# Optimization experiments

Measured on AMD Instinct MI355X. Metric: run time of the kernel, lower is better.

The kernel has to match this reference:

```python
import jax, jax.numpy as jnp
import numpy as np

WIDTH = 384
STEP_SIZE = 0.1  # hard-coded in EnergyBlock.__init__
EPS = 1e-5


def conv1d(x, w):
    # x: [B, Cin, L], w: [Cout, Cin, K], stride 1, SAME padding (padding=1 for k=3)
    return jax.lax.conv_general_dilated(
        x, w, window_strides=(1,), padding='SAME',
        dimension_numbers=('NCH', 'OIH', 'NCH'))


def layer_norm_cl(x):
    # torch layer_norm over shape[1:] == normalize jointly over (C, L) per batch elem,
    # no affine params, biased variance.
    mu = jnp.mean(x, axis=(1, 2), keepdims=True)
    var = jnp.mean(jnp.square(x - mu), axis=(1, 2), keepdims=True)
    return (x - mu) * jax.lax.rsqrt(var + EPS)


def energy_block(cat, op_w):
    # cat: [B, width+1, L] = concat(interim_thought, x)
    xl = layer_norm_cl(cat[:, :WIDTH])          # post-LN x (the grad variable)
    c = conv1d(cat, op_w)                        # operator(inputs): no path through xl
    # Ex = sum(c * xl) + sum(where(xl>=0, xl^2, 0))
    # dEx/dxl = c + 2*relu(xl)  (analytic; matches torch.autograd.grad)
    grads = c + 2.0 * jnp.maximum(xl, 0.0)
    return xl - STEP_SIZE * grads


def _init_conv(key, cout, cin, k=3):
    scale = (1.0 / (cin * k)) ** 0.5
    return jax.random.uniform(key, (cout, cin, k), jnp.float32, -scale, scale)


def setup_inputs() -> dict:
    key = jax.random.key(0)
    ks = jax.random.split(key, 6)
    B, L = 32, 512
    return {
        'x': jax.random.normal(ks[0], (B, 1, L), jnp.float32),
        'iters_to_do': 16,
        'proj_w': _init_conv(ks[1], WIDTH, 1),
        'op_w': _init_conv(ks[2], WIDTH, WIDTH + 1),
        'h1_w': _init_conv(ks[3], WIDTH, WIDTH),
        'h2_w': _init_conv(ks[4], WIDTH // 2, WIDTH),
        'h3_w': _init_conv(ks[5], 2, WIDTH // 2),
    }


def reference(x, iters_to_do, proj_w, op_w, h1_w, h2_w, h3_w):
    relu = jax.nn.relu
    interim = relu(conv1d(x, proj_w))  # initial_thought [B, width, L]

    def step(it, _):
        cat = jnp.concatenate([it, x], axis=1)       # recall=True
        new_it = energy_block(cat, op_w)
        out = conv1d(relu(conv1d(relu(conv1d(new_it, h1_w)), h2_w)), h3_w)  # [B,2,L]
        return new_it, out

    _, outs = jax.lax.scan(step, interim, None, length=iters_to_do)
    # eval mode: return all_outputs [B, iters, 2, L]
    return jnp.transpose(outs, (1, 0, 2, 3))
```

## Files before the change

### kernel.cpp

```cpp
#include <hip/hip_runtime.h>
#include <hip/hip_bf16.h>

#define BB 32
#define WW 384
#define LL 512
#define ITERS 16
#define NPB (WW * LL)
#define LROWS 514
#define RP (LROWS * 8)

typedef __attribute__((ext_vector_type(8))) short bf16x8;
typedef __attribute__((ext_vector_type(4))) float f32x4;

__device__ __forceinline__ float b2f(short s) {
    unsigned u = ((unsigned)(unsigned short)s) << 16;
    float f;
    __builtin_memcpy(&f, &u, 4);
    return f;
}
__device__ __forceinline__ short f2b(float v) {
    __hip_bfloat16 h = __float2bfloat16(v);
    return *(short*)&h;
}

__device__ __forceinline__ void gld16(const short* g, short* l) {
    __builtin_amdgcn_global_load_lds(
        (const __attribute__((address_space(1))) unsigned int*)g,
        (__attribute__((address_space(3))) unsigned int*)l, 16, 0, 0);
}

__global__ __launch_bounds__(256) void prep(
    const float* __restrict__ op_w, const float* __restrict__ h1_w,
    const float* __restrict__ h2_w, short* __restrict__ wOph,
    short* __restrict__ wH1, short* __restrict__ wH2, float* __restrict__ wx,
    short* itAh, short* itAl, short* itBh, short* itBl,
    short* a1A, short* a1B, short* a2A, short* a2B, float* part) {
    int bid = blockIdx.x, tid = threadIdx.x;
    if (bid < 1728) {
        int i = bid * 256 + tid;
        int e = i & 7, co = (i >> 3) % 384, oct = (i >> 3) / 384 % 48,
            tap = i / (8 * 384 * 48);
        wOph[i] = f2b(op_w[(co * 385 + oct * 8 + e) * 3 + tap]);
    } else if (bid < 3456) {
        int i = (bid - 1728) * 256 + tid;
        int e = i & 7, co = (i >> 3) % 384, oct = (i >> 3) / 384 % 48,
            tap = i / (8 * 384 * 48);
        wH1[i] = f2b(h1_w[(co * 384 + oct * 8 + e) * 3 + tap]);
    } else if (bid < 4320) {
        int i = (bid - 3456) * 256 + tid;
        int e = i & 7, co = (i >> 3) % 192, oct = (i >> 3) / 192 % 48,
            tap = i / (8 * 192 * 48);
        wH2[i] = f2b(h2_w[(co * 384 + oct * 8 + e) * 3 + tap]);
    } else if (bid < 4325) {
        int i = (bid - 4320) * 256 + tid;
        if (i < 3 * 384) {
            int co = i % 384, tap = i / 384;
            wx[tap * 384 + co] = op_w[(co * 385 + 384) * 3 + tap];
        }
    } else if (bid < 4330) {
        int i = (bid - 4325) * 256 + tid;
        if (i < (ITERS + 1) * 64) part[i] = 0.f;
    } else {
        int rb = bid - 4330;
        int row = (rb & 1) ? (LROWS - 1) : 0;
        int b = rb >> 1;
        for (int i = tid; i < 48 * 8; i += 256) {
            size_t o = (size_t)b * 48 * RP + (size_t)(i >> 3) * RP +
                       row * 8 + (i & 7);
            itAh[o] = 0; itAl[o] = 0; itBh[o] = 0; itBl[o] = 0;
            a1A[o] = 0; a1B[o] = 0;
        }
        for (int i = tid; i < 24 * 8; i += 256) {
            size_t o = (size_t)b * 24 * RP + (size_t)(i >> 3) * RP +
                       row * 8 + (i & 7);
            a2A[o] = 0; a2B[o] = 0;
        }
    }
}

__global__ __launch_bounds__(256) void proj_relu(const float* __restrict__ x,
                                                 const float* __restrict__ wp,
                                                 short* __restrict__ oh,
                                                 short* __restrict__ ol,
                                                 float* __restrict__ part) {
    int low3 = blockIdx.x & 7, r0 = blockIdx.x >> 3;
    int sl_lo = r0 & 3, chi = r0 >> 2;
    int c3 = chi * 8 + low3;
    int b = c3 >> 1, sl = ((c3 & 1) << 2) | sl_lo;
    int tid = threadIdx.x;
    __shared__ float ws[WW * 3];
    __shared__ float xs[66];
    for (int i = tid; i < WW * 3; i += 256) ws[i] = wp[i];
    int l0 = sl * 64;
    for (int i = tid; i < 66; i += 256) {
        int l = l0 + i - 1;
        xs[i] = (l >= 0 && l < LL) ? x[b * LL + l] : 0.f;
    }
    __syncthreads();
    size_t sb = (size_t)b * 48 * RP;
    float s = 0.f, sq = 0.f;
    for (int idx = tid; idx < 64 * WW; idx += 256) {
        int lo = idx / WW, co = idx % WW;
        float v = fmaxf(ws[co * 3] * xs[lo] + ws[co * 3 + 1] * xs[lo + 1] +
                            ws[co * 3 + 2] * xs[lo + 2], 0.f);
        size_t o = sb + (size_t)(co >> 3) * RP + (l0 + lo + 1) * 8 + (co & 7);
        __hip_bfloat16 h = __float2bfloat16(v);
        oh[o] = *(short*)&h;
        ol[o] = f2b(v - __bfloat162float(h));
        s += v; sq += v * v;
    }
    #pragma unroll
    for (int off = 32; off > 0; off >>= 1) {
        s += __shfl_down(s, off);
        sq += __shfl_down(sq, off);
    }
    __shared__ float sr[8];
    int w = tid >> 6;
    if ((tid & 63) == 0) { sr[w] = s; sr[4 + w] = sq; }
    __syncthreads();
    if (tid == 0) {
        atomicAdd(&part[b * 2], sr[0] + sr[1] + sr[2] + sr[3]);
        atomicAdd(&part[b * 2 + 1], sr[4] + sr[5] + sr[6] + sr[7]);
    }
}


#define PIPE_BARRIER()                                                     \
    do {                                                                   \
        asm volatile("s_waitcnt vmcnt(8)" ::: "memory");                   \
        __builtin_amdgcn_sched_barrier(0);                                 \
        __builtin_amdgcn_s_barrier();                                      \
        __builtin_amdgcn_sched_barrier(0);                                 \
    } while (0)

#define MMAC(A, B, MT, NT)                                                 \
    acc[MT][NT] = __builtin_amdgcn_mfma_f32_16x16x32_bf16(A, B,            \
                                                          acc[MT][NT], 0, 0, 0);

#define STAGE_R(KG, TB, S0, S1)                                            \
    do {                                                                   \
        short* sb_ = smem + (TB) * ASZ;                                    \
        _Pragma("unroll")                                                  \
        for (int r_ = 0; r_ < ((S1) - (S0) + 3) / 4; r_++) {               \
            int s_ = (S0) + r_ * 4 + wn;                                   \
            if (s_ < (S1)) {                                               \
                int u0_ = s_ * 64;                                         \
                if (u0_ > AU - 64) u0_ = AU - 64;                          \
                int u_ = u0_ + lane;                                       \
                int oc_ = u_ / TLROWS;                                     \
                int rw_ = u_ - oc_ * TLROWS;                               \
                gld16(inh + ibase + (size_t)((KG) * GOCT + oc_) * RP +     \
                          (size_t)(l0 + rw_) * 8,                          \
                      sb_ + u0_ * 8);                                      \
            }                                                              \
        }                                                                  \
    } while (0)

#define DECL_B(S) bf16x8 fb0##S, fb1##S, fb2##S, fb3##S;

#define LOADB(S, T, KC)                                                    \
    do {                                                                   \
        const short* bp_ = wh + ((((size_t)(T) * CHUNKS + (KC)) * 4 + q) * \
                                     COD + co0w + lane15) * 8;             \
        fb0##S = *(const bf16x8*)(bp_);                                    \
        fb1##S = *(const bf16x8*)(bp_ + 16 * 8);                           \
        fb2##S = *(const bf16x8*)(bp_ + 32 * 8);                           \
        fb3##S = *(const bf16x8*)(bp_ + 48 * 8);                           \
    } while (0)

#define COMP_TAP(SB, OG, T, S)                                             \
    do {                                                                   \
        const short* As_ = (SB);                                           \
        int ar_ = ((OG) * 4 + q) * TLROWS + wl + lane15 + (T);             \
        bf16x8 fa0 = *(const bf16x8*)(As_ + ar_ * 8);                      \
        bf16x8 fa1 = *(const bf16x8*)(As_ + (ar_ + 16) * 8);               \
        bf16x8 fa2 = *(const bf16x8*)(As_ + (ar_ + 32) * 8);               \
        bf16x8 fa3 = *(const bf16x8*)(As_ + (ar_ + 48) * 8);               \
        MMAC(fa0, fb0##S, 0, 0) MMAC(fa0, fb1##S, 0, 1)                    \
        MMAC(fa0, fb2##S, 0, 2) MMAC(fa0, fb3##S, 0, 3)                    \
        MMAC(fa1, fb0##S, 1, 0) MMAC(fa1, fb1##S, 1, 1)                    \
        MMAC(fa1, fb2##S, 1, 2) MMAC(fa1, fb3##S, 1, 3)                    \
        MMAC(fa2, fb0##S, 2, 0) MMAC(fa2, fb1##S, 2, 1)                    \
        MMAC(fa2, fb2##S, 2, 2) MMAC(fa2, fb3##S, 2, 3)                    \
        MMAC(fa3, fb0##S, 3, 0) MMAC(fa3, fb1##S, 3, 1)                    \
        MMAC(fa3, fb2##S, 3, 2) MMAC(fa3, fb3##S, 3, 3)                    \
    } while (0)

template <int CHUNKS, int IOCT, int OOCT, int COD, int MODE, int LSPLIT,
          int GOCT>
__device__ __forceinline__ void conv_body(
    int bid, short* smem,
    const short* __restrict__ inh, const short* __restrict__ inl,
    const short* __restrict__ wh, const float* __restrict__ xf,
    const float* __restrict__ wx, const float* __restrict__ part_in,
    float* __restrict__ part_out, short* __restrict__ outh,
    short* __restrict__ outl) {
    constexpr int TLROWS = LSPLIT ? 258 : 130;
    constexpr int SUBS = GOCT / 4;
    constexpr int NG = CHUNKS / SUBS;
    constexpr int ASZ = GOCT * TLROWS * 8;
    constexpr int AU = GOCT * TLROWS;
    constexpr int ANS = (AU + 63) / 64;
    constexpr int SPS = (ANS + SUBS - 1) / SUBS;

    int tid = threadIdx.x;
    int lane = tid & 63;
    int wn = __builtin_amdgcn_readfirstlane(tid >> 6);
    int lane15 = lane & 15, q = lane >> 4;
    int b, l0, co0, wl, wco;
    if (LSPLIT) {
        int low3 = bid & 7, r0 = bid >> 3;
        int ct = r0 % 3, chi = r0 / 3;
        int c2 = chi * 8 + low3;
        b = c2 >> 1; l0 = (c2 & 1) * 256; co0 = ct * 64;
        wl = wn * 64; wco = 0;
    } else {
        int low3 = bid & 7, r0 = bid >> 3;
        int ct = r0 % 3, s2 = r0 / 3;
        int ltlo = s2 & 1, chi = s2 >> 1;
        int c = chi * 8 + low3;
        b = c >> 1;
        int lt = ((c & 1) << 1) | ltlo;
        l0 = lt * 128; co0 = ct * 128;
        wl = (wn >> 1) * 64; wco = (wn & 1) * 64;
    }
    const int co0w = co0 + wco;
    const size_t ibase = (size_t)b * IOCT * RP;

    f32x4 acc[4][4];
    #pragma unroll
    for (int i = 0; i < 4; i++)
        #pragma unroll
        for (int j = 0; j < 4; j++) acc[i][j] = (f32x4){0.f, 0.f, 0.f, 0.f};

    DECL_B(X)
    DECL_B(Y)
    DECL_B(Z)
    STAGE_R(0, 0, 0, ANS);
    LOADB(X, 0, 0);
    LOADB(Y, 1, 0);
    PIPE_BARRIER();
    #pragma unroll 2
    for (int g = 0; g < NG; g++) {
        int cur = g & 1;
        short* sb = smem + cur * ASZ;
        #pragma unroll
        for (int s = 0; s < SUBS; s++) {
            int kc = g * SUBS + s;
            LOADB(Z, 2, kc);
            if (g + 1 < NG) {
                int s0 = s * SPS;
                int s1 = (s0 + SPS > ANS) ? ANS : s0 + SPS;
                STAGE_R(g + 1, cur ^ 1, s0, s1);
            }
            COMP_TAP(sb, s, 0, X);
            if (kc + 1 < CHUNKS) LOADB(X, 0, kc + 1);
            COMP_TAP(sb, s, 1, Y);
            if (kc + 1 < CHUNKS) LOADB(Y, 1, kc + 1);
            COMP_TAP(sb, s, 2, Z);
        }
        PIPE_BARRIER();
    }

    int l0w = l0 + wl;
    const size_t obase = (size_t)b * OOCT * RP;
    if constexpr (MODE == 1) {
        float s_in = part_in[b * 2], sq_in = part_in[b * 2 + 1];
        float mu = s_in / (float)NPB;
        float var = sq_in / (float)NPB - mu * mu;
        float rs = rsqrtf(var + 1e-5f);
        const float* xb = xf + b * LL;
        float s = 0.f, sq = 0.f;
        #pragma unroll
        for (int nt = 0; nt < 4; nt++) {
            int n = co0w + nt * 16 + lane15;
            float w0 = wx[n], w1 = wx[384 + n], w2 = wx[768 + n];
            #pragma unroll
            for (int mt = 0; mt < 4; mt++)
                #pragma unroll
                for (int r = 0; r < 4; r++) {
                    int m = mt * 16 + q * 4 + r;
                    int l = l0w + m;
                    size_t idx = ibase + (size_t)(n >> 3) * RP +
                                 (l + 1) * 8 + (n & 7);
                    float xm1 = (l > 0) ? xb[l - 1] : 0.f;
                    float xp1 = (l < LL - 1) ? xb[l + 1] : 0.f;
                    float c = acc[mt][nt][r] + w0 * xm1 + w1 * xb[l] + w2 * xp1;
                    float itv = b2f(inh[idx]) + b2f(inl[idx]);
                    float xl = (itv - mu) * rs;
                    float nv = xl - 0.1f * c - 0.2f * fmaxf(xl, 0.f);
                    s += nv;
                    sq += nv * nv;
                    __hip_bfloat16 h = __float2bfloat16(nv);
                    outh[idx] = *(short*)&h;
                    outl[idx] = f2b(nv - __bfloat162float(h));
                }
        }
        #pragma unroll
        for (int off = 32; off > 0; off >>= 1) {
            s += __shfl_down(s, off);
            sq += __shfl_down(sq, off);
        }
        __shared__ float sr[8];
        if (lane == 0) { sr[wn] = s; sr[4 + wn] = sq; }
        __syncthreads();
        if (tid == 0) {
            atomicAdd(&part_out[b * 2], sr[0] + sr[1] + sr[2] + sr[3]);
            atomicAdd(&part_out[b * 2 + 1], sr[4] + sr[5] + sr[6] + sr[7]);
        }
    } else {
        #pragma unroll
        for (int mt = 0; mt < 4; mt++)
            #pragma unroll
            for (int nt = 0; nt < 4; nt++)
                #pragma unroll
                for (int r = 0; r < 4; r++) {
                    int m = mt * 16 + q * 4 + r;
                    int n = co0w + nt * 16 + lane15;
                    size_t idx = obase + (size_t)(n >> 3) * RP +
                                 (l0w + m + 1) * 8 + (n & 7);
                    outh[idx] = f2b(fmaxf(acc[mt][nt][r], 0.f));
                }
    }
}

__device__ __forceinline__ void h3_body(int bid, short* smem,
                                        const short* __restrict__ a2,
                                        const float* __restrict__ w3,
                                        float* __restrict__ out, int t) {
    float* ws3 = (float*)smem;
    int tid = threadIdx.x;
    for (int i = tid; i < 2 * 192 * 3; i += 256) ws3[i] = w3[i];
    __syncthreads();
    int low3 = bid & 7, r0 = bid >> 3;
    int qlo = r0 & 1, chi = r0 >> 1;
    int c = chi * 8 + low3;
    int b = c >> 1;
    int qq = ((c & 1) << 1) | qlo;
    int l = qq * 128 + (tid >> 1);
    int ch = tid & 1;
    const short* ab = a2 + (size_t)b * 24 * RP;
    const float* wc = ws3 + ch * 576;
    float a = 0.f;
    #pragma unroll 4
    for (int oct = 0; oct < 24; oct++) {
        const short* p = ab + (size_t)oct * RP + l * 8;
        bf16x8 v0 = *(const bf16x8*)p;
        bf16x8 v1 = *(const bf16x8*)(p + 8);
        bf16x8 v2 = *(const bf16x8*)(p + 16);
        #pragma unroll
        for (int j = 0; j < 8; j++) {
            const float* wp = wc + (oct * 8 + j) * 3;
            a += wp[0] * b2f(v0[j]) + wp[1] * b2f(v1[j]) + wp[2] * b2f(v2[j]);
        }
    }
    out[(((size_t)b * ITERS + t) * 2 + ch) * LL + l] = a;
}

__global__ __launch_bounds__(256, 3) void fusedF(
    const short* __restrict__ ch, const short* __restrict__ cl,
    short* __restrict__ nh, short* __restrict__ nl,
    const short* __restrict__ wOph, const short* __restrict__ wH1,
    const short* __restrict__ wH2, const float* __restrict__ xf,
    const float* __restrict__ wx, const float* __restrict__ part_in,
    float* __restrict__ part_out, short* __restrict__ a1w,
    const short* __restrict__ a1r, short* __restrict__ a2w,
    const short* __restrict__ a2r, const float* __restrict__ w3,
    float* __restrict__ out, int th3, int opB, int h1B, int h2B) {
    __shared__ __align__(16) short smem[2 * 8 * 130 * 8];
    int bid = blockIdx.x;
    if (bid < opB) {
        conv_body<12, 48, 48, 384, 1, 0, 8>(bid, smem, ch, cl, wOph, xf, wx,
                                            part_in, part_out, nh, nl);
    } else if (bid < opB + h1B) {
        conv_body<12, 48, 48, 384, 0, 0, 8>(bid - opB, smem, ch, nullptr,
                                            wH1, nullptr, nullptr, nullptr,
                                            nullptr, a1w, nullptr);
    } else if (bid < opB + h1B + h2B) {
        conv_body<12, 48, 24, 192, 0, 1, 4>(bid - opB - h1B, smem, a1r,
                                            nullptr, wH2, nullptr, nullptr,
                                            nullptr, nullptr, a2w, nullptr);
    } else {
        h3_body(bid - opB - h1B - h2B, smem, a2r, w3, out, th3);
    }
}

extern "C" void kernel_launch(void* const* d_in, const int* in_sizes, int n_in,
                              void* d_out, int out_size, void* d_ws, size_t ws_size,
                              hipStream_t stream) {
    const float* x = (const float*)d_in[0];
    const float* proj_w = (const float*)d_in[2];
    const float* op_w = (const float*)d_in[3];
    const float* h1_w = (const float*)d_in[4];
    const float* h2_w = (const float*)d_in[5];
    const float* h3_w = (const float*)d_in[6];
    float* out = (float*)d_out;

    char* base = (char*)d_ws;
    size_t off = 0;
    auto alloc = [&](size_t bytes) {
        char* p = base + off;
        off += (bytes + 255) & ~(size_t)255;
        return p;
    };
    const size_t ITB = (size_t)BB * 48 * RP * 2;
    short* itAh = (short*)alloc(ITB);
    short* itAl = (short*)alloc(ITB);
    short* itBh = (short*)alloc(ITB);
    short* itBl = (short*)alloc(ITB);
    short* a1A = (short*)alloc((size_t)BB * 48 * RP * 2);
    short* a1B = (short*)alloc((size_t)BB * 48 * RP * 2);
    short* a2A = (short*)alloc((size_t)BB * 24 * RP * 2);
    short* a2B = (short*)alloc((size_t)BB * 24 * RP * 2);
    short* wOph = (short*)alloc((size_t)3 * 48 * 384 * 8 * 2);
    short* wH1 = (short*)alloc((size_t)3 * 48 * 384 * 8 * 2);
    short* wH2 = (short*)alloc((size_t)3 * 48 * 192 * 8 * 2);
    float* wx = (float*)alloc((size_t)3 * 384 * 4);
    float* part = (float*)alloc((size_t)(ITERS + 1) * 64 * 4);
    if (off > ws_size) return;

    prep<<<4394, 256, 0, stream>>>(op_w, h1_w, h2_w, wOph, wH1, wH2, wx,
                                   itAh, itAl, itBh, itBl, a1A, a1B, a2A,
                                   a2B, part);
    proj_relu<<<BB * 8, 256, 0, stream>>>(x, proj_w, itAh, itAl, part);

    short* a1buf[2] = {a1A, a1B};
    short* a2buf[2] = {a2A, a2B};
    short *ch = itAh, *cl = itAl, *nh = itBh, *nl = itBl;
    for (int t = 0; t < ITERS + 3; t++) {
        int opB = (t < ITERS) ? 384 : 0;
        int h1B = (t >= 1 && t <= ITERS) ? 384 : 0;
        int h2B = (t >= 2 && t <= ITERS + 1) ? 192 : 0;
        int h3B = (t >= 3 && t <= ITERS + 2) ? 128 : 0;
        int tp = (t < ITERS) ? t : 0;
        fusedF<<<opB + h1B + h2B + h3B, 256, 0, stream>>>(
            ch, cl, nh, nl, wOph, wH1, wH2, x, wx, part + tp * 64,
            part + (tp + 1) * 64, a1buf[(t - 1) & 1], a1buf[(t - 2) & 1],
            a2buf[(t - 2) & 1], a2buf[(t + 1) & 1], h3_w, out, t - 3,
            opB, h1B, h2B);
        if (t < ITERS) {
            short* th = ch; ch = nh; nh = th;
            short* tl = cl; cl = nl; nl = tl;
        }
    }
}
```

Baseline: 940.4 us.

## Shrink LDS staging to 4-octet chunks and unify h2 tiling with op/h1

```diff
diff --git a/kernel.cpp b/kernel.cpp
--- a/kernel.cpp
+++ b/kernel.cpp
@@ -137,19 +137,19 @@
     acc[MT][NT] = __builtin_amdgcn_mfma_f32_16x16x32_bf16(A, B,            \
                                                           acc[MT][NT], 0, 0, 0);
 
-#define STAGE_R(KG, TB, S0, S1)                                            \
+#define STAGE(KC, TB)                                                      \
     do {                                                                   \
         short* sb_ = smem + (TB) * ASZ;                                    \
         _Pragma("unroll")                                                  \
-        for (int r_ = 0; r_ < ((S1) - (S0) + 3) / 4; r_++) {               \
-            int s_ = (S0) + r_ * 4 + wn;                                   \
-            if (s_ < (S1)) {                                               \
+        for (int r_ = 0; r_ < 3; r_++) {                                   \
+            int s_ = r_ * 4 + wn;                                          \
+            if (s_ < 9) {                                                  \
                 int u0_ = s_ * 64;                                         \
                 if (u0_ > AU - 64) u0_ = AU - 64;                          \
                 int u_ = u0_ + lane;                                       \
                 int oc_ = u_ / TLROWS;                                     \
                 int rw_ = u_ - oc_ * TLROWS;                               \
-                gld16(inh + ibase + (size_t)((KG) * GOCT + oc_) * RP +     \
+                gld16(inh + ibase + (size_t)((KC) * 4 + oc_) * RP +        \
                           (size_t)(l0 + rw_) * 8,                          \
                       sb_ + u0_ * 8);                                      \
             }                                                              \
@@ -168,10 +168,10 @@
         fb3##S = *(const bf16x8*)(bp_ + 48 * 8);                           \
     } while (0)
 
-#define COMP_TAP(SB, OG, T, S)                                             \
+#define COMP_TAP(SB, T, S)                                                 \
     do {                                                                   \
         const short* As_ = (SB);                                           \
-        int ar_ = ((OG) * 4 + q) * TLROWS + wl + lane15 + (T);             \
+        int ar_ = q * TLROWS + wl + lane15 + (T);                          \
         bf16x8 fa0 = *(const bf16x8*)(As_ + ar_ * 8);                      \
         bf16x8 fa1 = *(const bf16x8*)(As_ + (ar_ + 16) * 8);               \
         bf16x8 fa2 = *(const bf16x8*)(As_ + (ar_ + 32) * 8);               \
@@ -186,8 +186,8 @@
         MMAC(fa3, fb2##S, 3, 2) MMAC(fa3, fb3##S, 3, 3)                    \
     } while (0)
 
-template <int CHUNKS, int IOCT, int OOCT, int COD, int MODE, int LSPLIT,
-          int GOCT>
+template <int CHUNKS, int IOCT, int OOCT, int COD, int MODE, int NCT,
+          int CSTR>
 __device__ __forceinline__ void conv_body(
     int bid, short* smem,
     const short* __restrict__ inh, const short* __restrict__ inl,
@@ -195,35 +195,22 @@
     const float* __restrict__ wx, const float* __restrict__ part_in,
     float* __restrict__ part_out, short* __restrict__ outh,
     short* __restrict__ outl) {
-    constexpr int TLROWS = LSPLIT ? 258 : 130;
-    constexpr int SUBS = GOCT / 4;
-    constexpr int NG = CHUNKS / SUBS;
-    constexpr int ASZ = GOCT * TLROWS * 8;
-    constexpr int AU = GOCT * TLROWS;
-    constexpr int ANS = (AU + 63) / 64;
-    constexpr int SPS = (ANS + SUBS - 1) / SUBS;
+    constexpr int TLROWS = 130;
+    constexpr int ASZ = 4 * TLROWS * 8;
+    constexpr int AU = 4 * TLROWS;
 
     int tid = threadIdx.x;
     int lane = tid & 63;
     int wn = __builtin_amdgcn_readfirstlane(tid >> 6);
     int lane15 = lane & 15, q = lane >> 4;
-    int b, l0, co0, wl, wco;
-    if (LSPLIT) {
-        int low3 = bid & 7, r0 = bid >> 3;
-        int ct = r0 % 3, chi = r0 / 3;
-        int c2 = chi * 8 + low3;
-        b = c2 >> 1; l0 = (c2 & 1) * 256; co0 = ct * 64;
-        wl = wn * 64; wco = 0;
-    } else {
-        int low3 = bid & 7, r0 = bid >> 3;
-        int ct = r0 % 3, s2 = r0 / 3;
-        int ltlo = s2 & 1, chi = s2 >> 1;
-        int c = chi * 8 + low3;
-        b = c >> 1;
-        int lt = ((c & 1) << 1) | ltlo;
-        l0 = lt * 128; co0 = ct * 128;
-        wl = (wn >> 1) * 64; wco = (wn & 1) * 64;
-    }
+    int low3 = bid & 7, r0 = bid >> 3;
+    int ct = r0 % NCT, s2 = r0 / NCT;
+    int ltlo = s2 & 1, chi = s2 >> 1;
+    int c = chi * 8 + low3;
+    int b = c >> 1;
+    int lt = ((c & 1) << 1) | ltlo;
+    int l0 = lt * 128, co0 = ct * CSTR;
+    int wl = (wn >> 1) * 64, wco = (wn & 1) * 64;
     const int co0w = co0 + wco;
     const size_t ibase = (size_t)b * IOCT * RP;
 
@@ -236,29 +223,21 @@
     DECL_B(X)
     DECL_B(Y)
     DECL_B(Z)
-    STAGE_R(0, 0, 0, ANS);
+    STAGE(0, 0);
     LOADB(X, 0, 0);
     LOADB(Y, 1, 0);
     PIPE_BARRIER();
     #pragma unroll 2
-    for (int g = 0; g < NG; g++) {
-        int cur = g & 1;
+    for (int kc = 0; kc < CHUNKS; kc++) {
+        int cur = kc & 1;
+        LOADB(Z, 2, kc);
+        if (kc + 1 < CHUNKS) STAGE(kc + 1, cur ^ 1);
         short* sb = smem + cur * ASZ;
-        #pragma unroll
-        for (int s = 0; s < SUBS; s++) {
-            int kc = g * SUBS + s;
-            LOADB(Z, 2, kc);
-            if (g + 1 < NG) {
-                int s0 = s * SPS;
-                int s1 = (s0 + SPS > ANS) ? ANS : s0 + SPS;
-                STAGE_R(g + 1, cur ^ 1, s0, s1);
-            }
-            COMP_TAP(sb, s, 0, X);
-            if (kc + 1 < CHUNKS) LOADB(X, 0, kc + 1);
-            COMP_TAP(sb, s, 1, Y);
-            if (kc + 1 < CHUNKS) LOADB(Y, 1, kc + 1);
-            COMP_TAP(sb, s, 2, Z);
-        }
+        COMP_TAP(sb, 0, X);
+        if (kc + 1 < CHUNKS) LOADB(X, 0, kc + 1);
+        COMP_TAP(sb, 1, Y);
+        if (kc + 1 < CHUNKS) LOADB(Y, 1, kc + 1);
+        COMP_TAP(sb, 2, Z);
         PIPE_BARRIER();
     }
 
@@ -285,10 +264,11 @@
                                  (l + 1) * 8 + (n & 7);
                     float xm1 = (l > 0) ? xb[l - 1] : 0.f;
                     float xp1 = (l < LL - 1) ? xb[l + 1] : 0.f;
-                    float c = acc[mt][nt][r] + w0 * xm1 + w1 * xb[l] + w2 * xp1;
+                    float c2 = acc[mt][nt][r] + w0 * xm1 + w1 * xb[l] +
+                               w2 * xp1;
                     float itv = b2f(inh[idx]) + b2f(inl[idx]);
                     float xl = (itv - mu) * rs;
-                    float nv = xl - 0.1f * c - 0.2f * fmaxf(xl, 0.f);
+                    float nv = xl - 0.1f * c2 - 0.2f * fmaxf(xl, 0.f);
                     s += nv;
                     sq += nv * nv;
                     __hip_bfloat16 h = __float2bfloat16(nv);
@@ -357,7 +337,7 @@
     out[(((size_t)b * ITERS + t) * 2 + ch) * LL + l] = a;
 }
 
-__global__ __launch_bounds__(256, 3) void fusedF(
+__global__ __launch_bounds__(256, 4) void fusedF(
     const short* __restrict__ ch, const short* __restrict__ cl,
     short* __restrict__ nh, short* __restrict__ nl,
     const short* __restrict__ wOph, const short* __restrict__ wH1,
@@ -367,19 +347,19 @@
     const short* __restrict__ a1r, short* __restrict__ a2w,
     const short* __restrict__ a2r, const float* __restrict__ w3,
     float* __restrict__ out, int th3, int opB, int h1B, int h2B) {
-    __shared__ __align__(16) short smem[2 * 8 * 130 * 8];
+    __shared__ __align__(16) short smem[2 * 4 * 130 * 8];
     int bid = blockIdx.x;
     if (bid < opB) {
-        conv_body<12, 48, 48, 384, 1, 0, 8>(bid, smem, ch, cl, wOph, xf, wx,
-                                            part_in, part_out, nh, nl);
+        conv_body<12, 48, 48, 384, 1, 3, 128>(bid, smem, ch, cl, wOph, xf,
+                                              wx, part_in, part_out, nh, nl);
     } else if (bid < opB + h1B) {
-        conv_body<12, 48, 48, 384, 0, 0, 8>(bid - opB, smem, ch, nullptr,
-                                            wH1, nullptr, nullptr, nullptr,
-                                            nullptr, a1w, nullptr);
+        conv_body<12, 48, 48, 384, 0, 3, 128>(bid - opB, smem, ch, nullptr,
+                                              wH1, nullptr, nullptr, nullptr,
+                                              nullptr, a1w, nullptr);
     } else if (bid < opB + h1B + h2B) {
-        conv_body<12, 48, 24, 192, 0, 1, 4>(bid - opB - h1B, smem, a1r,
-                                            nullptr, wH2, nullptr, nullptr,
-                                            nullptr, nullptr, a2w, nullptr);
+        conv_body<12, 48, 24, 192, 0, 2, 64>(bid - opB - h1B, smem, a1r,
+                                             nullptr, wH2, nullptr, nullptr,
+                                             nullptr, nullptr, a2w, nullptr);
     } else {
         h3_body(bid - opB - h1B - h2B, smem, a2r, w3, out, th3);
     }
@@ -430,7 +410,7 @@
     for (int t = 0; t < ITERS + 3; t++) {
         int opB = (t < ITERS) ? 384 : 0;
         int h1B = (t >= 1 && t <= ITERS) ? 384 : 0;
-        int h2B = (t >= 2 && t <= ITERS + 1) ? 192 : 0;
+        int h2B = (t >= 2 && t <= ITERS + 1) ? 256 : 0;
         int h3B = (t >= 3 && t <= ITERS + 2) ? 128 : 0;
         int tp = (t < ITERS) ? t : 0;
         fusedF<<<opB + h1B + h2B + h3B, 256, 0, stream>>>(
```

New measurement: 1.413 ms. +50.2%, slower.

## Fuse h3 conv into h2 conv epilogue with atomic output accumulation

Applied to the files above, without the earlier changes.

```diff
diff --git a/kernel.cpp b/kernel.cpp
--- a/kernel.cpp
+++ b/kernel.cpp
@@ -34,7 +34,7 @@
     const float* __restrict__ h2_w, short* __restrict__ wOph,
     short* __restrict__ wH1, short* __restrict__ wH2, float* __restrict__ wx,
     short* itAh, short* itAl, short* itBh, short* itBl,
-    short* a1A, short* a1B, short* a2A, short* a2B, float* part) {
+    short* a1A, short* a1B, float* part, float* outz) {
     int bid = blockIdx.x, tid = threadIdx.x;
     if (bid < 1728) {
         int i = bid * 256 + tid;
@@ -60,7 +60,7 @@
     } else if (bid < 4330) {
         int i = (bid - 4325) * 256 + tid;
         if (i < (ITERS + 1) * 64) part[i] = 0.f;
-    } else {
+    } else if (bid < 4394) {
         int rb = bid - 4330;
         int row = (rb & 1) ? (LROWS - 1) : 0;
         int b = rb >> 1;
@@ -70,11 +70,9 @@
             itAh[o] = 0; itAl[o] = 0; itBh[o] = 0; itBl[o] = 0;
             a1A[o] = 0; a1B[o] = 0;
         }
-        for (int i = tid; i < 24 * 8; i += 256) {
-            size_t o = (size_t)b * 24 * RP + (size_t)(i >> 3) * RP +
-                       row * 8 + (i & 7);
-            a2A[o] = 0; a2B[o] = 0;
-        }
+    } else {
+        int i = (bid - 4394) * 256 + tid;
+        outz[i] = 0.f;
     }
 }
 
@@ -189,12 +187,13 @@
 template <int CHUNKS, int IOCT, int OOCT, int COD, int MODE, int LSPLIT,
           int GOCT>
 __device__ __forceinline__ void conv_body(
-    int bid, short* smem,
+    int bid, short* smem, float* ws3s,
     const short* __restrict__ inh, const short* __restrict__ inl,
     const short* __restrict__ wh, const float* __restrict__ xf,
     const float* __restrict__ wx, const float* __restrict__ part_in,
     float* __restrict__ part_out, short* __restrict__ outh,
-    short* __restrict__ outl) {
+    short* __restrict__ outl, const float* __restrict__ w3p,
+    float* __restrict__ outp, int th) {
     constexpr int TLROWS = LSPLIT ? 258 : 130;
     constexpr int SUBS = GOCT / 4;
     constexpr int NG = CHUNKS / SUBS;
@@ -308,6 +307,63 @@
             atomicAdd(&part_out[b * 2], sr[0] + sr[1] + sr[2] + sr[3]);
             atomicAdd(&part_out[b * 2 + 1], sr[4] + sr[5] + sr[6] + sr[7]);
         }
+    } else if constexpr (MODE == 2) {
+        short* a2loc = smem;
+        #pragma unroll
+        for (int mt = 0; mt < 4; mt++)
+            #pragma unroll
+            for (int nt = 0; nt < 4; nt++)
+                #pragma unroll
+                for (int r = 0; r < 4; r++) {
+                    int row = wl + mt * 16 + q * 4 + r + 1;
+                    int cl = nt * 16 + lane15;
+                    a2loc[(cl >> 3) * (258 * 8) + row * 8 + (cl & 7)] =
+                        f2b(fmaxf(acc[mt][nt][r], 0.f));
+                }
+        if (wn < 2) {
+            int le = (wn == 0) ? (l0 - 1) : (l0 + 256);
+            int rowdst = (wn == 0) ? 0 : 257;
+            float s = 0.f;
+            if (le >= 0 && le < LL) {
+                int cog = co0 + lane;
+                #pragma unroll 2
+                for (int oc = 0; oc < 48; oc++) {
+                    const short* ap = inh + ibase + (size_t)oc * RP + le * 8;
+                    #pragma unroll
+                    for (int tp = 0; tp < 3; tp++) {
+                        bf16x8 av = *(const bf16x8*)(ap + tp * 8);
+                        const short* wp =
+                            wh + ((size_t)(tp * 48 + oc) * COD + cog) * 8;
+                        #pragma unroll
+                        for (int j = 0; j < 8; j++)
+                            s += b2f(av[j]) * b2f(wp[j]);
+                    }
+                }
+                s = fmaxf(s, 0.f);
+            }
+            a2loc[(lane >> 3) * (258 * 8) + rowdst * 8 + (lane & 7)] = f2b(s);
+        }
+        for (int i = tid; i < 2 * 192 * 3; i += 256) ws3s[i] = w3p[i];
+        __syncthreads();
+        int ll = tid;
+        float s0 = 0.f, s1 = 0.f;
+        #pragma unroll 2
+        for (int cil = 0; cil < 64; cil++) {
+            int cig = co0 + cil;
+            const float* wp0 = ws3s + cig * 3;
+            const float* wp1 = ws3s + 576 + cig * 3;
+            const short* ap = a2loc + (cil >> 3) * (258 * 8) + ll * 8 +
+                              (cil & 7);
+            #pragma unroll
+            for (int tp = 0; tp < 3; tp++) {
+                float av = b2f(ap[tp * 8]);
+                s0 += wp0[tp] * av;
+                s1 += wp1[tp] * av;
+            }
+        }
+        float* ob = outp + (((size_t)b * ITERS + th) * 2) * LL + l0 + ll;
+        atomicAdd(ob, s0);
+        atomicAdd(ob + LL, s1);
     } else {
         #pragma unroll
         for (int mt = 0; mt < 4; mt++)
@@ -324,39 +380,6 @@
     }
 }
 
-__device__ __forceinline__ void h3_body(int bid, short* smem,
-                                        const short* __restrict__ a2,
-                                        const float* __restrict__ w3,
-                                        float* __restrict__ out, int t) {
-    float* ws3 = (float*)smem;
-    int tid = threadIdx.x;
-    for (int i = tid; i < 2 * 192 * 3; i += 256) ws3[i] = w3[i];
-    __syncthreads();
-    int low3 = bid & 7, r0 = bid >> 3;
-    int qlo = r0 & 1, chi = r0 >> 1;
-    int c = chi * 8 + low3;
-    int b = c >> 1;
-    int qq = ((c & 1) << 1) | qlo;
-    int l = qq * 128 + (tid >> 1);
-    int ch = tid & 1;
-    const short* ab = a2 + (size_t)b * 24 * RP;
-    const float* wc = ws3 + ch * 576;
-    float a = 0.f;
-    #pragma unroll 4
-    for (int oct = 0; oct < 24; oct++) {
-        const short* p = ab + (size_t)oct * RP + l * 8;
-        bf16x8 v0 = *(const bf16x8*)p;
-        bf16x8 v1 = *(const bf16x8*)(p + 8);
-        bf16x8 v2 = *(const bf16x8*)(p + 16);
-        #pragma unroll
-        for (int j = 0; j < 8; j++) {
-            const float* wp = wc + (oct * 8 + j) * 3;
-            a += wp[0] * b2f(v0[j]) + wp[1] * b2f(v1[j]) + wp[2] * b2f(v2[j]);
-        }
-    }
-    out[(((size_t)b * ITERS + t) * 2 + ch) * LL + l] = a;
-}
-
 __global__ __launch_bounds__(256, 3) void fusedF(
     const short* __restrict__ ch, const short* __restrict__ cl,
     short* __restrict__ nh, short* __restrict__ nl,
@@ -364,24 +387,25 @@
     const short* __restrict__ wH2, const float* __restrict__ xf,
     const float* __restrict__ wx, const float* __restrict__ part_in,
     float* __restrict__ part_out, short* __restrict__ a1w,
-    const short* __restrict__ a1r, short* __restrict__ a2w,
-    const short* __restrict__ a2r, const float* __restrict__ w3,
-    float* __restrict__ out, int th3, int opB, int h1B, int h2B) {
+    const short* __restrict__ a1r, const float* __restrict__ w3,
+    float* __restrict__ out, int th, int opB, int h1B) {
     __shared__ __align__(16) short smem[2 * 8 * 130 * 8];
+    __shared__ float ws3s[2 * 192 * 3];
     int bid = blockIdx.x;
     if (bid < opB) {
-        conv_body<12, 48, 48, 384, 1, 0, 8>(bid, smem, ch, cl, wOph, xf, wx,
-                                            part_in, part_out, nh, nl);
+        conv_body<12, 48, 48, 384, 1, 0, 8>(bid, smem, ws3s, ch, cl, wOph,
+                                            xf, wx, part_in, part_out, nh,
+                                            nl, nullptr, nullptr, 0);
     } else if (bid < opB + h1B) {
-        conv_body<12, 48, 48, 384, 0, 0, 8>(bid - opB, smem, ch, nullptr,
-                                            wH1, nullptr, nullptr, nullptr,
-                                            nullptr, a1w, nullptr);
-    } else if (bid < opB + h1B + h2B) {
-        conv_body<12, 48, 24, 192, 0, 1, 4>(bid - opB - h1B, smem, a1r,
-                                            nullptr, wH2, nullptr, nullptr,
-                                            nullptr, nullptr, a2w, nullptr);
+        conv_body<12, 48, 48, 384, 0, 0, 8>(bid - opB, smem, ws3s, ch,
+                                            nullptr, wH1, nullptr, nullptr,
+                                            nullptr, nullptr, a1w, nullptr,
+                                            nullptr, nullptr, 0);
     } else {
-        h3_body(bid - opB - h1B - h2B, smem, a2r, w3, out, th3);
+        conv_body<12, 48, 24, 192, 2, 1, 4>(bid - opB - h1B, smem, ws3s,
+                                            a1r, nullptr, wH2, nullptr,
+                                            nullptr, nullptr, nullptr,
+                                            nullptr, nullptr, w3, out, th);
     }
 }
 
@@ -410,8 +434,6 @@
     short* itBl = (short*)alloc(ITB);
     short* a1A = (short*)alloc((size_t)BB * 48 * RP * 2);
     short* a1B = (short*)alloc((size_t)BB * 48 * RP * 2);
-    short* a2A = (short*)alloc((size_t)BB * 24 * RP * 2);
-    short* a2B = (short*)alloc((size_t)BB * 24 * RP * 2);
     short* wOph = (short*)alloc((size_t)3 * 48 * 384 * 8 * 2);
     short* wH1 = (short*)alloc((size_t)3 * 48 * 384 * 8 * 2);
     short* wH2 = (short*)alloc((size_t)3 * 48 * 192 * 8 * 2);
@@ -419,25 +441,22 @@
     float* part = (float*)alloc((size_t)(ITERS + 1) * 64 * 4);
     if (off > ws_size) return;
 
-    prep<<<4394, 256, 0, stream>>>(op_w, h1_w, h2_w, wOph, wH1, wH2, wx,
-                                   itAh, itAl, itBh, itBl, a1A, a1B, a2A,
-                                   a2B, part);
+    prep<<<6442, 256, 0, stream>>>(op_w, h1_w, h2_w, wOph, wH1, wH2, wx,
+                                   itAh, itAl, itBh, itBl, a1A, a1B, part,
+                                   out);
     proj_relu<<<BB * 8, 256, 0, stream>>>(x, proj_w, itAh, itAl, part);
 
     short* a1buf[2] = {a1A, a1B};
-    short* a2buf[2] = {a2A, a2B};
     short *ch = itAh, *cl = itAl, *nh = itBh, *nl = itBl;
-    for (int t = 0; t < ITERS + 3; t++) {
+    for (int t = 0; t < ITERS + 2; t++) {
         int opB = (t < ITERS) ? 384 : 0;
         int h1B = (t >= 1 && t <= ITERS) ? 384 : 0;
         int h2B = (t >= 2 && t <= ITERS + 1) ? 192 : 0;
-        int h3B = (t >= 3 && t <= ITERS + 2) ? 128 : 0;
         int tp = (t < ITERS) ? t : 0;
-        fusedF<<<opB + h1B + h2B + h3B, 256, 0, stream>>>(
+        fusedF<<<opB + h1B + h2B, 256, 0, stream>>>(
             ch, cl, nh, nl, wOph, wH1, wH2, x, wx, part + tp * 64,
             part + (tp + 1) * 64, a1buf[(t - 1) & 1], a1buf[(t - 2) & 1],
-            a2buf[(t - 2) & 1], a2buf[(t + 1) & 1], h3_w, out, t - 3,
-            opB, h1B, h2B);
+            h3_w, out, t - 2, opB, h1B);
         if (t < ITERS) {
             short* th = ch; ch = nh; nh = th;
             short* tl = cl; cl = nl; nl = tl;
```

After: 1.121 ms. 19.2% more time.
